# Performance work log

Measured on AMD Instinct MI355X. Metric: run time of the kernel, lower is better.

## Reference

```python
import jax, jax.numpy as jnp
import numpy as np

C = 512
NH = 8
DH = 64
GROUPS = 8
EPS = 1e-5


def setup_inputs() -> dict:
    key = jax.random.key(0)
    ks = jax.random.split(key, 20)
    s = 0.02
    d = {
        'x': jax.random.normal(ks[0], (16, C, 32, 32), jnp.float32),
        'gn_w': jnp.ones((C,), jnp.float32),
        'gn_b': jnp.zeros((C,), jnp.float32),
        'pin_w': jax.random.normal(ks[1], (C, C), jnp.float32) * s,
        'pin_b': jnp.zeros((C,), jnp.float32),
        'ln1_w': jnp.ones((C,), jnp.float32),
        'ln1_b': jnp.zeros((C,), jnp.float32),
        'wq': jax.random.normal(ks[2], (C, C), jnp.float32) * s,
        'wk': jax.random.normal(ks[3], (C, C), jnp.float32) * s,
        'wv': jax.random.normal(ks[4], (C, C), jnp.float32) * s,
        'wo': jax.random.normal(ks[5], (C, C), jnp.float32) * s,
        'bo': jnp.zeros((C,), jnp.float32),
        'ln3_w': jnp.ones((C,), jnp.float32),
        'ln3_b': jnp.zeros((C,), jnp.float32),
        'wg': jax.random.normal(ks[6], (C, 8 * C), jnp.float32) * s,
        'bg': jnp.zeros((8 * C,), jnp.float32),
        'wd': jax.random.normal(ks[7], (4 * C, C), jnp.float32) * s,
        'bd': jnp.zeros((C,), jnp.float32),
        'pout_w': jax.random.normal(ks[8], (C, C), jnp.float32) * s,
        'pout_b': jnp.zeros((C,), jnp.float32),
    }
    return d


def _group_norm(x, w, b):
    B, Cc, H, W = x.shape
    xg = x.reshape(B, GROUPS, Cc // GROUPS, H, W)
    mu = xg.mean(axis=(2, 3, 4), keepdims=True)
    var = xg.var(axis=(2, 3, 4), keepdims=True)
    xn = ((xg - mu) * jax.lax.rsqrt(var + EPS)).reshape(B, Cc, H, W)
    return xn * w[None, :, None, None] + b[None, :, None, None]


def _layer_norm(x, w, b):
    mu = x.mean(axis=-1, keepdims=True)
    var = x.var(axis=-1, keepdims=True)
    return (x - mu) * jax.lax.rsqrt(var + EPS) * w + b


def reference(x, gn_w, gn_b, pin_w, pin_b, ln1_w, ln1_b, wq, wk, wv, wo, bo,
              ln3_w, ln3_b, wg, bg, wd, bd, pout_w, pout_b):
    B, Cc, H, W = x.shape
    x_in = x
    h = _group_norm(x, gn_w, gn_b)
    # proj_in: 1x1 conv == channel matmul
    h = jnp.einsum('bchw,oc->bohw', h, pin_w) + pin_b[None, :, None, None]
    # [B, S, C] tokens
    t = h.reshape(B, Cc, H * W).transpose(0, 2, 1)
    # --- attention block ---
    tn = _layer_norm(t, ln1_w, ln1_b)
    S = H * W
    q = (tn @ wq).reshape(B, S, NH, DH)
    k = (tn @ wk).reshape(B, S, NH, DH)
    v = (tn @ wv).reshape(B, S, NH, DH)
    scale = DH ** -0.5
    scores = jnp.einsum('bshd,bthd->bhst', q, k) * scale  # [B,NH,S,S]
    wts = jax.nn.softmax(scores, axis=-1)
    attn = jnp.einsum('bhst,bthd->bshd', wts, v).reshape(B, S, Cc)
    t = attn @ wo + bo + t
    # --- GEGLU MLP ---
    tn = _layer_norm(t, ln3_w, ln3_b)
    hp = tn @ wg + bg
    a, g = hp[..., :4 * Cc], hp[..., 4 * Cc:]
    t = (a * jax.nn.gelu(g, approximate=False)) @ wd + bd + t
    # back to image
    h = t.transpose(0, 2, 1).reshape(B, Cc, H, W)
    out = jnp.einsum('bchw,oc->bohw', h, pout_w) + pout_b[None, :, None, None]
    return out + x_in
```

## Files before the change

### kernel.cpp

```cpp
#include <hip/hip_runtime.h>
#include <hip/hip_bf16.h>
#include <math.h>

typedef unsigned short u16;
typedef __attribute__((ext_vector_type(8))) short bf16x8;
typedef __attribute__((ext_vector_type(4))) float f32x4;

#define Bb 16
#define Cch 512
#define Ss 1024
#define NHh 8
#define DHh 64
#define CPG 64
#define EPSV 1e-5f
#define R_TOTAL (Bb*Ss)
#define QSCL 0.18033688011112042f

__device__ inline u16 f2bf(float f) {
    unsigned int u = __float_as_uint(f);
    unsigned int r = (u + 0x7fffu + ((u >> 16) & 1u)) >> 16;
    return (u16)r;
}
__device__ inline u16 f2bf_rz(float f) { return (u16)(__float_as_uint(f) >> 16); }
__device__ inline float bf2f(u16 v) { return __uint_as_float((unsigned)v << 16); }
__device__ inline float exp2_raw(float x) {
    float r; asm("v_exp_f32 %0, %1" : "=v"(r) : "v"(x)); return r;
}
__device__ inline float rcp_raw(float x) {
    float r; asm("v_rcp_f32 %0, %1" : "=v"(r) : "v"(x)); return r;
}
__device__ inline float gelu_f(float g) {
    float z = fabsf(g) * 0.70710678118654752f;
    float t = rcp_raw(1.0f + 0.3275911f * z);
    float poly = t * (0.254829592f + t * (-0.284496736f + t * (1.421413741f +
                 t * (-1.453152027f + t * 1.061405429f))));
    float e = exp2_raw(-z * z * 1.44269504089f);
    float erfa = 1.0f - poly * e;
    float erfv = (g < 0.f) ? -erfa : erfa;
    return 0.5f * g * (1.0f + erfv);
}

__device__ inline int swz(int row, int chunk) {
    return row * 64 + ((chunk ^ (row & 7)) * 8);
}
__device__ inline int psw(int row, int chunk) {
    return ((chunk >> 3) << 13) + row * 64 + (((chunk & 7) ^ (row & 7)) * 8);
}
__device__ inline int vsw(int row, int chunk) {
    return ((chunk >> 3) << 12) + row * 64 + (((chunk & 7) ^ (row & 7)) * 8);
}
__device__ inline int swzg(int r, int c) {
    int span = r >> 1;
    int c8 = ((r & 1) << 2) | c;
    return span * 64 + ((c8 ^ (span & 7)) * 8);
}

__global__ __launch_bounds__(256) void gn_stats(const float* __restrict__ x,
                                                float* __restrict__ stats) {
    int bg = blockIdx.x;
    int b = bg >> 3, g = bg & 7;
    const float4* base = (const float4*)(x + ((size_t)b * Cch + (size_t)g * CPG) * Ss);
    float s = 0.f, ss = 0.f;
    for (int i = threadIdx.x; i < CPG * Ss / 4; i += 256) {
        float4 v = base[i];
        s  += v.x + v.y + v.z + v.w;
        ss += v.x * v.x + v.y * v.y + v.z * v.z + v.w * v.w;
    }
    for (int o = 32; o > 0; o >>= 1) { s += __shfl_down(s, o); ss += __shfl_down(ss, o); }
    __shared__ float red[2][4];
    int wid = threadIdx.x >> 6, lane = threadIdx.x & 63;
    if (lane == 0) { red[0][wid] = s; red[1][wid] = ss; }
    __syncthreads();
    if (threadIdx.x == 0) {
        float S1 = red[0][0] + red[0][1] + red[0][2] + red[0][3];
        float S2 = red[1][0] + red[1][1] + red[1][2] + red[1][3];
        const float inv_n = 1.0f / (CPG * Ss);
        float mu = S1 * inv_n;
        float var = S2 * inv_n - mu * mu;
        stats[bg * 2]     = mu;
        stats[bg * 2 + 1] = rsqrtf(var + EPSV);
    }
}

__global__ __launch_bounds__(256) void gn_apply_t_bf(const float* __restrict__ x,
                                                     const float* __restrict__ stats,
                                                     const float* __restrict__ gw,
                                                     const float* __restrict__ gb,
                                                     u16* __restrict__ ht) {
    __shared__ float tile[32][33];
    int b  = blockIdx.z;
    int c0 = blockIdx.y * 32;
    int s0 = blockIdx.x * 32;
    int tx = threadIdx.x, ty = threadIdx.y;
#pragma unroll
    for (int i = 0; i < 4; i++) {
        int c = c0 + ty + i * 8;
        int g = c >> 6;
        float mu = stats[(b * 8 + g) * 2];
        float rs = stats[(b * 8 + g) * 2 + 1];
        float v = x[((size_t)b * Cch + c) * Ss + s0 + tx];
        tile[ty + i * 8][tx] = (v - mu) * rs * gw[c] + gb[c];
    }
    __syncthreads();
#pragma unroll
    for (int i = 0; i < 4; i++) {
        int s = s0 + ty + i * 8;
        ht[((size_t)b * Ss + s) * Cch + c0 + tx] = f2bf(tile[tx][ty + i * 8]);
    }
}

__global__ __launch_bounds__(256) void prep_all(const float* __restrict__ pin_w,
                                                const float* __restrict__ pout_w,
                                                u16* __restrict__ pinB,
                                                u16* __restrict__ poutB,
                                                const float* __restrict__ wq,
                                                const float* __restrict__ wk,
                                                const float* __restrict__ wv,
                                                const float* __restrict__ wo,
                                                u16* __restrict__ wqT,
                                                u16* __restrict__ wkT,
                                                u16* __restrict__ wvT,
                                                u16* __restrict__ woT,
                                                const float* __restrict__ wg,
                                                u16* __restrict__ wgT,
                                                const float* __restrict__ wd,
                                                u16* __restrict__ wdT) {
    __shared__ float tile[32][33];
    int bid = blockIdx.x;
    int tx = threadIdx.x, ty = threadIdx.y;
    int tid = ty * 32 + tx;
    if (bid < 512) {
        int base = bid * 1024 + tid * 4;
        const float* src; u16* dst; int off;
        if (base < 262144) { src = pin_w;  dst = pinB;  off = base; }
        else               { src = pout_w; dst = poutB; off = base - 262144; }
        float4 v = *(const float4*)&src[off];
        ushort4 o;
        o.x = f2bf(v.x); o.y = f2bf(v.y); o.z = f2bf(v.z); o.w = f2bf(v.w);
        *(ushort4*)&dst[off] = o;
        return;
    }
    const float* in; u16* outp; int c0, r0, C, R; float scl = 1.0f;
    if (bid < 1536) {
        int z = (bid - 512) >> 8, rem = (bid - 512) & 255;
        switch (z) {
            case 0: in = wq; outp = wqT; scl = QSCL; break;
            case 1: in = wk; outp = wkT; break;
            case 2: in = wv; outp = wvT; break;
            default: in = wo; outp = woT; break;
        }
        c0 = (rem & 15) * 32; r0 = (rem >> 4) * 32; C = 512; R = 512;
    } else if (bid < 3584) {
        int rem = bid - 1536;
        in = wg; outp = wgT; C = 4096; R = 512;
        c0 = (rem & 127) * 32; r0 = (rem >> 7) * 32;
    } else {
        int rem = bid - 3584;
        in = wd; outp = wdT; C = 512; R = 2048;
        c0 = (rem & 15) * 32; r0 = (rem >> 4) * 32;
    }
#pragma unroll
    for (int i = 0; i < 4; i++)
        tile[ty + i * 8][tx] = in[(size_t)(r0 + ty + i * 8) * C + c0 + tx] * scl;
    __syncthreads();
#pragma unroll
    for (int i = 0; i < 4; i++)
        outp[(size_t)(c0 + ty + i * 8) * R + r0 + tx] = f2bf(tile[tx][ty + i * 8]);
}

__global__ __launch_bounds__(256) void vtrans(const u16* __restrict__ in,
                                              u16* __restrict__ outp) {
    __shared__ u16 tile[64][66];
    int s0 = blockIdx.x * 64, h = blockIdx.y, b = blockIdx.z;
    const u16* src = in + ((size_t)b * Ss + s0) * Cch + h * 64;
    int r = threadIdx.x >> 3, c8 = (threadIdx.x & 7) * 8;
#pragma unroll
    for (int p = 0; p < 2; p++) {
        int rr = r + p * 32;
        *(int4*)&tile[rr][c8] = *(const int4*)&src[(size_t)rr * Cch + c8];
    }
    __syncthreads();
    u16* dst = outp + ((size_t)(b * 8 + h) * 64) * Ss + s0;
#pragma unroll
    for (int p = 0; p < 2; p++) {
        int d = r + p * 32;
        u16 vals[8];
#pragma unroll
        for (int e = 0; e < 8; e++) vals[e] = tile[c8 + e][d];
        *(int4*)&dst[(size_t)d * Ss + c8] = *(int4*)vals;
    }
}

__global__ __launch_bounds__(256) void layer_norm_rows_bf(const u16* __restrict__ in,
                                                          const float* __restrict__ w,
                                                          const float* __restrict__ bb,
                                                          u16* __restrict__ outp) {
    int row = blockIdx.x;
    const u16* p = in + (size_t)row * Cch;
    int i0 = threadIdx.x * 2;
    ushort2 u = *(const ushort2*)&p[i0];
    float v0 = bf2f(u.x), v1 = bf2f(u.y);
    float s = v0 + v1, ss = v0 * v0 + v1 * v1;
    for (int o = 32; o > 0; o >>= 1) { s += __shfl_down(s, o); ss += __shfl_down(ss, o); }
    __shared__ float red[2][4];
    __shared__ float mu_s, rs_s;
    int wid = threadIdx.x >> 6, lane = threadIdx.x & 63;
    if (lane == 0) { red[0][wid] = s; red[1][wid] = ss; }
    __syncthreads();
    if (threadIdx.x == 0) {
        float S1 = red[0][0] + red[0][1] + red[0][2] + red[0][3];
        float S2 = red[1][0] + red[1][1] + red[1][2] + red[1][3];
        float mu = S1 * (1.0f / Cch);
        float var = S2 * (1.0f / Cch) - mu * mu;
        mu_s = mu; rs_s = rsqrtf(var + EPSV);
    }
    __syncthreads();
    float mu = mu_s, rs = rs_s;
    outp[(size_t)row * Cch + i0]     = f2bf((v0 - mu) * rs * w[i0] + bb[i0]);
    outp[(size_t)row * Cch + i0 + 1] = f2bf((v1 - mu) * rs * w[i0 + 1] + bb[i0 + 1]);
}

template<int EPI>
__global__ __launch_bounds__(512) void mfma_gemm(const u16* __restrict__ A,
                                                 const u16* __restrict__ Bt,
                                                 const float* __restrict__ bias,
                                                 float* __restrict__ fout,
                                                 u16* __restrict__ outb,
                                                 int K, int N) {
    __shared__ u16 As[256 * 32];
    __shared__ u16 Bs[128 * 32];
    int tid = threadIdx.x;
    int m0 = blockIdx.y * 256, n0 = blockIdx.x * 128;
    int wave = tid >> 6, lane = tid & 63;
    int wr = wave >> 1, wc = wave & 1;
    int l15 = lane & 15, l4 = lane >> 4;

    f32x4 zero4 = {0.f, 0.f, 0.f, 0.f};
    f32x4 acc[4][4];
#pragma unroll
    for (int i = 0; i < 4; i++)
#pragma unroll
        for (int j = 0; j < 4; j++) acc[i][j] = zero4;

    int srow = tid >> 1;
    int sc0  = (tid & 1) * 2;
    int se   = sc0 * 8;
    int brow = tid >> 2;
    int bch  = tid & 3;
    int bqe  = bch * 8;

    int4 ra0, ra1, rb0;
    {
        const u16* pa = A  + (size_t)(m0 + srow) * K + se;
        ra0 = *(const int4*)pa; ra1 = *(const int4*)(pa + 8);
        rb0 = *(const int4*)(Bt + (size_t)(n0 + brow) * K + bqe);
    }
    for (int kt = 0; kt < K; kt += 32) {
        __syncthreads();
        *(int4*)&As[swzg(srow, sc0)]     = ra0;
        *(int4*)&As[swzg(srow, sc0 + 1)] = ra1;
        *(int4*)&Bs[swzg(brow, bch)]     = rb0;
        __syncthreads();
        int kn = kt + 32;
        if (kn < K) {
            const u16* pa = A  + (size_t)(m0 + srow) * K + kn + se;
            ra0 = *(const int4*)pa; ra1 = *(const int4*)(pa + 8);
            rb0 = *(const int4*)(Bt + (size_t)(n0 + brow) * K + kn + bqe);
        }
        bf16x8 af[4], bfr[4];
#pragma unroll
        for (int mi = 0; mi < 4; mi++)
            af[mi] = *(const bf16x8*)&As[swzg(wr * 64 + mi * 16 + l15, l4)];
#pragma unroll
        for (int nj = 0; nj < 4; nj++)
            bfr[nj] = *(const bf16x8*)&Bs[swzg(wc * 64 + nj * 16 + l15, l4)];
#pragma unroll
        for (int mi = 0; mi < 4; mi++)
#pragma unroll
            for (int nj = 0; nj < 4; nj++)
                acc[mi][nj] = __builtin_amdgcn_mfma_f32_16x16x32_bf16(af[mi], bfr[nj], acc[mi][nj], 0, 0, 0);
    }

#pragma unroll
    for (int mi = 0; mi < 4; mi++)
#pragma unroll
        for (int nj = 0; nj < 4; nj++)
#pragma unroll
            for (int r = 0; r < 4; r++) {
                int row = m0 + wr * 64 + mi * 16 + l4 * 4 + r;
                int col = n0 + wc * 64 + nj * 16 + l15;
                float v = acc[mi][nj][r];
                if constexpr (EPI == 0) {
                    outb[(size_t)row * N + col] = f2bf(v);
                } else if constexpr (EPI == 1) {
                    fout[(size_t)row * N + col] = v + bias[col];
                } else if constexpr (EPI == 6) {
                    outb[(size_t)row * N + col] = f2bf(v + bias[col]);
                } else if constexpr (EPI == 7) {
                    size_t idx = (size_t)row * N + col;
                    v += bias[col] + bf2f(outb[idx]);
                    outb[idx] = f2bf(v);
                } else if constexpr (EPI == 8) {
                    size_t idx = (size_t)(col >> 9) * 8388608 + (size_t)row * 512 + (col & 511);
                    outb[idx] = f2bf(v);
                }
            }
}

__global__ __launch_bounds__(512) void geglu_mfma(const u16* __restrict__ A,
                                                  const u16* __restrict__ WgT,
                                                  const float* __restrict__ bg,
                                                  u16* __restrict__ ag) {
    __shared__ u16 As[256 * 32];
    __shared__ u16 Bs1[64 * 32];
    __shared__ u16 Bs2[64 * 32];
    const int K = 512;
    int tid = threadIdx.x;
    int m0 = blockIdx.y * 256, n0 = blockIdx.x * 64;
    int wave = tid >> 6, lane = tid & 63;
    int wr = wave >> 1, wc = wave & 1;
    int l15 = lane & 15, l4 = lane >> 4;

    f32x4 zero4 = {0.f, 0.f, 0.f, 0.f};
    f32x4 accA[4][2], accG[4][2];
#pragma unroll
    for (int i = 0; i < 4; i++) { accA[i][0] = zero4; accA[i][1] = zero4; accG[i][0] = zero4; accG[i][1] = zero4; }

    int srow = tid >> 1;
    int sc0  = (tid & 1) * 2;
    int se   = sc0 * 8;
    int bsel = tid >> 8;
    int bt   = tid & 255;
    int brow = bt >> 2;
    int bch  = bt & 3;
    int bqe  = bch * 8;
    const u16* gbp = WgT + (size_t)(bsel * 2048 + n0 + brow) * K + bqe;

    int4 ra0, ra1, rb;
    {
        const u16* pa = A + (size_t)(m0 + srow) * K + se;
        ra0 = *(const int4*)pa; ra1 = *(const int4*)(pa + 8);
        rb = *(const int4*)gbp;
    }
    for (int kt = 0; kt < K; kt += 32) {
        __syncthreads();
        *(int4*)&As[swzg(srow, sc0)]     = ra0;
        *(int4*)&As[swzg(srow, sc0 + 1)] = ra1;
        if (bsel == 0) *(int4*)&Bs1[swzg(brow, bch)] = rb;
        else           *(int4*)&Bs2[swzg(brow, bch)] = rb;
        __syncthreads();
        int kn = kt + 32;
        if (kn < K) {
            const u16* pa = A + (size_t)(m0 + srow) * K + kn + se;
            ra0 = *(const int4*)pa; ra1 = *(const int4*)(pa + 8);
            rb = *(const int4*)(gbp + kn);
        }
        bf16x8 af[4], b1[2], b2[2];
#pragma unroll
        for (int mi = 0; mi < 4; mi++)
            af[mi] = *(const bf16x8*)&As[swzg(wr * 64 + mi * 16 + l15, l4)];
#pragma unroll
        for (int nj = 0; nj < 2; nj++) {
            b1[nj] = *(const bf16x8*)&Bs1[swzg(wc * 32 + nj * 16 + l15, l4)];
            b2[nj] = *(const bf16x8*)&Bs2[swzg(wc * 32 + nj * 16 + l15, l4)];
        }
#pragma unroll
        for (int mi = 0; mi < 4; mi++)
#pragma unroll
            for (int nj = 0; nj < 2; nj++) {
                accA[mi][nj] = __builtin_amdgcn_mfma_f32_16x16x32_bf16(af[mi], b1[nj], accA[mi][nj], 0, 0, 0);
                accG[mi][nj] = __builtin_amdgcn_mfma_f32_16x16x32_bf16(af[mi], b2[nj], accG[mi][nj], 0, 0, 0);
            }
    }

#pragma unroll
    for (int mi = 0; mi < 4; mi++)
#pragma unroll
        for (int nj = 0; nj < 2; nj++)
#pragma unroll
            for (int r = 0; r < 4; r++) {
                int row = m0 + wr * 64 + mi * 16 + l4 * 4 + r;
                int col = n0 + wc * 32 + nj * 16 + l15;
                float a = accA[mi][nj][r] + bg[col];
                float g = accG[mi][nj][r] + bg[2048 + col];
                ag[(size_t)row * 2048 + col] = f2bf(a * gelu_f(g));
            }
}

__global__ __launch_bounds__(512) void flash_attn_mfma(const u16* __restrict__ q,
                                                       const u16* __restrict__ k,
                                                       const u16* __restrict__ vt,
                                                       u16* __restrict__ o) {
    __shared__ u16 Ps[2 * 128 * 64];
    __shared__ u16 Ks[128 * 64];
    __shared__ u16 Vt[2 * 64 * 64];
    const int tid = threadIdx.x;
    const int h = blockIdx.x, b = blockIdx.z;
    const int q0 = blockIdx.y * 128;
    const size_t hb  = (size_t)b * Ss * Cch + (size_t)h * DHh;
    const size_t vhb = ((size_t)(b * NHh + h) * DHh) * Ss;

    const int wq = tid >> 6;
    const int lane = tid & 63;
    const int l15 = lane & 15, l4 = lane >> 4;

    const int kr = tid >> 2, kc = (tid & 3) * 2;
    const int vf = tid >> 8, vtn = tid & 255;
    const int vd = vtn >> 2, vc = (vtn & 3) * 2;
    const u16* kbase = k + hb + (size_t)kr * Cch + (size_t)kc * 8;
    const u16* vbase = vt + vhb + (size_t)vd * Ss + vf * 64 + (size_t)vc * 8;

    {
        int r = tid >> 2, ch = (tid & 3) * 2;
        const u16* src = q + hb + (size_t)(q0 + r) * Cch;
        *(int4*)&Ps[psw(r, ch)]     = *(const int4*)(src + ch * 8);
        *(int4*)&Ps[psw(r, ch + 1)] = *(const int4*)(src + (ch + 1) * 8);
    }
    __syncthreads();
    bf16x8 aq[2];
    aq[0] = *(const bf16x8*)&Ps[psw(wq * 16 + l15, 0 * 4 + l4)];
    aq[1] = *(const bf16x8*)&Ps[psw(wq * 16 + l15, 1 * 4 + l4)];

    f32x4 zero4 = {0.f, 0.f, 0.f, 0.f};
    f32x4 oacc[4];
    float m_[4], l_[4];
#pragma unroll
    for (int j = 0; j < 4; j++) oacc[j] = zero4;
#pragma unroll
    for (int r = 0; r < 4; r++) { m_[r] = -1e30f; l_[r] = 0.f; }

    int4 rk0, rk1, rv0, rv1;
    rk0 = *(const int4*)(kbase);
    rk1 = *(const int4*)(kbase + 8);
    rv0 = *(const int4*)(vbase);
    rv1 = *(const int4*)(vbase + 8);

    for (int t0 = 0; t0 < Ss; t0 += 128) {
        __syncthreads();
        *(int4*)&Ks[swz(kr, kc)]     = rk0;
        *(int4*)&Ks[swz(kr, kc + 1)] = rk1;
        *(int4*)&Vt[vsw(vd, vf * 8 + vc)]     = rv0;
        *(int4*)&Vt[vsw(vd, vf * 8 + vc + 1)] = rv1;
        __syncthreads();
        if (t0 + 128 < Ss) {
            rk0 = *(const int4*)(kbase + (size_t)(t0 + 128) * Cch);
            rk1 = *(const int4*)(kbase + (size_t)(t0 + 128) * Cch + 8);
            rv0 = *(const int4*)(vbase + t0 + 128);
            rv1 = *(const int4*)(vbase + t0 + 128 + 8);
        }

        f32x4 sacc[8];
#pragma unroll
        for (int j = 0; j < 8; j++) sacc[j] = zero4;
#pragma unroll
        for (int ks = 0; ks < 2; ks++) {
#pragma unroll
            for (int j = 0; j < 8; j++) {
                bf16x8 bk = *(const bf16x8*)&Ks[swz(j * 16 + l15, ks * 4 + l4)];
                sacc[j] = __builtin_amdgcn_mfma_f32_16x16x32_bf16(aq[ks], bk, sacc[j], 0, 0, 0);
            }
        }

        float tmv[4];
        int grew = 0;
#pragma unroll
        for (int r = 0; r < 4; r++) {
            float tm = fmaxf(fmaxf(fmaxf(sacc[0][r], sacc[1][r]), fmaxf(sacc[2][r], sacc[3][r])),
                             fmaxf(fmaxf(sacc[4][r], sacc[5][r]), fmaxf(sacc[6][r], sacc[7][r])));
            tm = fmaxf(tm, __shfl_xor(tm, 1));
            tm = fmaxf(tm, __shfl_xor(tm, 2));
            tm = fmaxf(tm, __shfl_xor(tm, 4));
            tm = fmaxf(tm, __shfl_xor(tm, 8));
            tmv[r] = tm;
            grew |= (tm > m_[r]);
        }

        if (__any(grew)) {
#pragma unroll
            for (int r = 0; r < 4; r++) {
                float nm = fmaxf(m_[r], tmv[r]);
                float sc = exp2_raw(m_[r] - nm);
                m_[r] = nm;
                int row = wq * 16 + l4 * 4 + r;
                int rx = row & 7, b64 = row * 64, wi = l15 & 7, hi = l15 >> 3;
                float rs = 0.f;
#pragma unroll
                for (int j = 0; j < 8; j++) {
                    float p = exp2_raw(sacc[j][r] - nm);
                    int cnk = 2 * j + hi;
                    Ps[((cnk >> 3) << 13) + b64 + (((cnk & 7) ^ rx) * 8) + wi] = f2bf_rz(p);
                    rs += p;
                }
                l_[r] = l_[r] * sc + rs;
#pragma unroll
                for (int j = 0; j < 4; j++) oacc[j][r] *= sc;
            }
        } else {
#pragma unroll
            for (int r = 0; r < 4; r++) {
                float nm = m_[r];
                int row = wq * 16 + l4 * 4 + r;
                int rx = row & 7, b64 = row * 64, wi = l15 & 7, hi = l15 >> 3;
                float rs = 0.f;
#pragma unroll
                for (int j = 0; j < 8; j++) {
                    float p = exp2_raw(sacc[j][r] - nm);
                    int cnk = 2 * j + hi;
                    Ps[((cnk >> 3) << 13) + b64 + (((cnk & 7) ^ rx) * 8) + wi] = f2bf_rz(p);
                    rs += p;
                }
                l_[r] += rs;
            }
        }

#pragma unroll
        for (int ks = 0; ks < 4; ks++) {
            bf16x8 pa = *(const bf16x8*)&Ps[psw(wq * 16 + l15, ks * 4 + l4)];
#pragma unroll
            for (int j = 0; j < 4; j++) {
                bf16x8 bv = *(const bf16x8*)&Vt[vsw(j * 16 + l15, ks * 4 + l4)];
                oacc[j] = __builtin_amdgcn_mfma_f32_16x16x32_bf16(pa, bv, oacc[j], 0, 0, 0);
            }
        }
    }

#pragma unroll
    for (int r = 0; r < 4; r++) {
        float lt = l_[r];
        lt += __shfl_xor(lt, 1);
        lt += __shfl_xor(lt, 2);
        lt += __shfl_xor(lt, 4);
        lt += __shfl_xor(lt, 8);
        float inv = 1.0f / lt;
        int row = wq * 16 + l4 * 4 + r;
        int rx = row & 7, b64 = row * 64, wi = l15 & 7, hi = l15 >> 3;
#pragma unroll
        for (int j = 0; j < 4; j++) {
            int cnk = 2 * j + hi;
            Ps[b64 + ((cnk ^ rx) * 8) + wi] = f2bf(oacc[j][r] * inv);
        }
    }
    __syncthreads();
    {
        int r = tid >> 2, ch = (tid & 3) * 2;
        u16* dst = o + hb + (size_t)(q0 + r) * Cch;
        *(int4*)(dst + ch * 8)       = *(const int4*)&Ps[psw(r, ch)];
        *(int4*)(dst + (ch + 1) * 8) = *(const int4*)&Ps[psw(r, ch + 1)];
    }
}

__global__ __launch_bounds__(256) void final_out_bf(const u16* __restrict__ tmp,
                                                    const float* __restrict__ x,
                                                    float* __restrict__ outp) {
    __shared__ float tile[32][33];
    int b = blockIdx.z, c0 = blockIdx.y * 32, s0 = blockIdx.x * 32;
    int tx = threadIdx.x, ty = threadIdx.y;
#pragma unroll
    for (int i = 0; i < 4; i++) {
        int s = s0 + ty + i * 8;
        tile[ty + i * 8][tx] = bf2f(tmp[((size_t)b * Ss + s) * Cch + c0 + tx]);
    }
    __syncthreads();
#pragma unroll
    for (int i = 0; i < 4; i++) {
        int c = c0 + ty + i * 8;
        size_t idx = ((size_t)b * Cch + c) * Ss + s0 + tx;
        outp[idx] = tile[tx][ty + i * 8] + x[idx];
    }
}

extern "C" void kernel_launch(void* const* d_in, const int* in_sizes, int n_in,
                              void* d_out, int out_size, void* d_ws, size_t ws_size,
                              hipStream_t stream) {
    (void)in_sizes; (void)n_in; (void)out_size; (void)ws_size;
    const float* x      = (const float*)d_in[0];
    const float* gn_w   = (const float*)d_in[1];
    const float* gn_b   = (const float*)d_in[2];
    const float* pin_w  = (const float*)d_in[3];
    const float* pin_b  = (const float*)d_in[4];
    const float* ln1_w  = (const float*)d_in[5];
    const float* ln1_b  = (const float*)d_in[6];
    const float* wq     = (const float*)d_in[7];
    const float* wk     = (const float*)d_in[8];
    const float* wv     = (const float*)d_in[9];
    const float* wo     = (const float*)d_in[10];
    const float* bo     = (const float*)d_in[11];
    const float* ln3_w  = (const float*)d_in[12];
    const float* ln3_b  = (const float*)d_in[13];
    const float* wg     = (const float*)d_in[14];
    const float* bg     = (const float*)d_in[15];
    const float* wd     = (const float*)d_in[16];
    const float* bd     = (const float*)d_in[17];
    const float* pout_w = (const float*)d_in[18];
    const float* pout_b = (const float*)d_in[19];
    float* out = (float*)d_out;

    char* W = (char*)d_ws;
    u16* tb        = (u16*)W;
    float* tmp_f32 = (float*)(W + 33554432);
    u16* qb    = (u16*)(W + 67108864);
    u16* kb    = qb + 8388608;
    u16* vb    = kb + 8388608;
    u16* attnb = vb + 8388608;
    u16* Xb    = attnb + 8388608;
    float* stats = (float*)(W + 67108864 + 5ull * 16777216);
    u16* wbase = (u16*)(W + 67108864 + 5ull * 16777216 + 1024);
    u16* pinB  = wbase;
    u16* poutB = pinB  + 262144;
    u16* wqT   = poutB + 262144;
    u16* wkT   = wqT   + 262144;
    u16* wvT   = wkT   + 262144;
    u16* woT   = wvT   + 262144;
    u16* wgT   = woT   + 262144;
    u16* wdT   = wgT   + 2097152;
    u16* ag    = qb;
    u16* vtb   = (u16*)tmp_f32;

    dim3 tb8(32, 8);

    gn_stats<<<128, 256, 0, stream>>>(x, stats);
    prep_all<<<4608, tb8, 0, stream>>>(pin_w, pout_w, pinB, poutB,
                                       wq, wk, wv, wo, wqT, wkT, wvT, woT,
                                       wg, wgT, wd, wdT);

    gn_apply_t_bf<<<dim3(32, 16, 16), tb8, 0, stream>>>(x, stats, gn_w, gn_b, Xb);

    mfma_gemm<6><<<dim3(4, 64), 512, 0, stream>>>(Xb, pinB, pin_b, nullptr, tb, 512, 512);
    layer_norm_rows_bf<<<16384, 256, 0, stream>>>(tb, ln1_w, ln1_b, Xb);
    mfma_gemm<8><<<dim3(12, 64), 512, 0, stream>>>(Xb, wqT, nullptr, nullptr, qb, 512, 1536);
    vtrans<<<dim3(16, 8, 16), 256, 0, stream>>>(vb, vtb);
    flash_attn_mfma<<<dim3(8, 8, 16), 512, 0, stream>>>(qb, kb, vtb, attnb);
    mfma_gemm<7><<<dim3(4, 64), 512, 0, stream>>>(attnb, woT, bo, nullptr, tb, 512, 512);
    layer_norm_rows_bf<<<16384, 256, 0, stream>>>(tb, ln3_w, ln3_b, Xb);
    geglu_mfma<<<dim3(32, 64), 512, 0, stream>>>(Xb, wgT, bg, ag);
    mfma_gemm<7><<<dim3(4, 64), 512, 0, stream>>>(ag, wdT, bd, nullptr, tb, 2048, 512);
    mfma_gemm<6><<<dim3(4, 64), 512, 0, stream>>>(tb, poutB, pout_b, nullptr, Xb, 512, 512);
    final_out_bf<<<dim3(32, 16, 16), tb8, 0, stream>>>(Xb, x, out);
}
```

Before: 422.0 us.

## Double-buffer shared memory tiles in MFMA GEMM to drop a barrier per k-step

```diff
diff --git a/kernel.cpp b/kernel.cpp
--- a/kernel.cpp
+++ b/kernel.cpp
@@ -227,8 +227,8 @@
                                                  float* __restrict__ fout,
                                                  u16* __restrict__ outb,
                                                  int K, int N) {
-    __shared__ u16 As[256 * 32];
-    __shared__ u16 Bs[128 * 32];
+    __shared__ u16 As[2][256 * 32];
+    __shared__ u16 Bs[2][128 * 32];
     int tid = threadIdx.x;
     int m0 = blockIdx.y * 256, n0 = blockIdx.x * 128;
     int wave = tid >> 6, lane = tid & 63;
@@ -249,36 +249,46 @@
     int bch  = tid & 3;
     int bqe  = bch * 8;
 
-    int4 ra0, ra1, rb0;
-    {
-        const u16* pa = A  + (size_t)(m0 + srow) * K + se;
-        ra0 = *(const int4*)pa; ra1 = *(const int4*)(pa + 8);
-        rb0 = *(const int4*)(Bt + (size_t)(n0 + brow) * K + bqe);
-    }
+    const u16* pa = A  + (size_t)(m0 + srow) * K + se;
+    const u16* pb = Bt + (size_t)(n0 + brow) * K + bqe;
+
+    int4 ra0 = *(const int4*)pa;
+    int4 ra1 = *(const int4*)(pa + 8);
+    int4 rb0 = *(const int4*)pb;
+    *(int4*)&As[0][swzg(srow, sc0)]     = ra0;
+    *(int4*)&As[0][swzg(srow, sc0 + 1)] = ra1;
+    *(int4*)&Bs[0][swzg(brow, bch)]     = rb0;
+    ra0 = *(const int4*)(pa + 32);
+    ra1 = *(const int4*)(pa + 40);
+    rb0 = *(const int4*)(pb + 32);
+    __syncthreads();
+
+    int p = 0;
     for (int kt = 0; kt < K; kt += 32) {
-        __syncthreads();
-        *(int4*)&As[swzg(srow, sc0)]     = ra0;
-        *(int4*)&As[swzg(srow, sc0 + 1)] = ra1;
-        *(int4*)&Bs[swzg(brow, bch)]     = rb0;
-        __syncthreads();
-        int kn = kt + 32;
-        if (kn < K) {
-            const u16* pa = A  + (size_t)(m0 + srow) * K + kn + se;
-            ra0 = *(const int4*)pa; ra1 = *(const int4*)(pa + 8);
-            rb0 = *(const int4*)(Bt + (size_t)(n0 + brow) * K + kn + bqe);
-        }
         bf16x8 af[4], bfr[4];
 #pragma unroll
         for (int mi = 0; mi < 4; mi++)
-            af[mi] = *(const bf16x8*)&As[swzg(wr * 64 + mi * 16 + l15, l4)];
+            af[mi] = *(const bf16x8*)&As[p][swzg(wr * 64 + mi * 16 + l15, l4)];
 #pragma unroll
         for (int nj = 0; nj < 4; nj++)
-            bfr[nj] = *(const bf16x8*)&Bs[swzg(wc * 64 + nj * 16 + l15, l4)];
+            bfr[nj] = *(const bf16x8*)&Bs[p][swzg(wc * 64 + nj * 16 + l15, l4)];
 #pragma unroll
         for (int mi = 0; mi < 4; mi++)
 #pragma unroll
             for (int nj = 0; nj < 4; nj++)
                 acc[mi][nj] = __builtin_amdgcn_mfma_f32_16x16x32_bf16(af[mi], bfr[nj], acc[mi][nj], 0, 0, 0);
+        if (kt + 32 < K) {
+            *(int4*)&As[p ^ 1][swzg(srow, sc0)]     = ra0;
+            *(int4*)&As[p ^ 1][swzg(srow, sc0 + 1)] = ra1;
+            *(int4*)&Bs[p ^ 1][swzg(brow, bch)]     = rb0;
+            if (kt + 64 < K) {
+                ra0 = *(const int4*)(pa + kt + 64);
+                ra1 = *(const int4*)(pa + kt + 72);
+                rb0 = *(const int4*)(pb + kt + 64);
+            }
+        }
+        __syncthreads();
+        p ^= 1;
     }
 
 #pragma unroll
```

New measurement: 406.2 us. 3.7% less time.

## Double-buffer LDS tiles in MFMA GEMM with two-stage register prefetch

Applied to the files above, without the earlier changes.

```diff
diff --git a/kernel.cpp b/kernel.cpp
--- a/kernel.cpp
+++ b/kernel.cpp
@@ -221,14 +221,14 @@
 }
 
 template<int EPI>
-__global__ __launch_bounds__(512) void mfma_gemm(const u16* __restrict__ A,
-                                                 const u16* __restrict__ Bt,
-                                                 const float* __restrict__ bias,
-                                                 float* __restrict__ fout,
-                                                 u16* __restrict__ outb,
-                                                 int K, int N) {
-    __shared__ u16 As[256 * 32];
-    __shared__ u16 Bs[128 * 32];
+__global__ __launch_bounds__(512, 2) void mfma_gemm(const u16* __restrict__ A,
+                                                    const u16* __restrict__ Bt,
+                                                    const float* __restrict__ bias,
+                                                    float* __restrict__ fout,
+                                                    u16* __restrict__ outb,
+                                                    int K, int N) {
+    __shared__ u16 As[2][256 * 32];
+    __shared__ u16 Bs[2][128 * 32];
     int tid = threadIdx.x;
     int m0 = blockIdx.y * 256, n0 = blockIdx.x * 128;
     int wave = tid >> 6, lane = tid & 63;
@@ -249,36 +249,72 @@
     int bch  = tid & 3;
     int bqe  = bch * 8;
 
-    int4 ra0, ra1, rb0;
-    {
-        const u16* pa = A  + (size_t)(m0 + srow) * K + se;
-        ra0 = *(const int4*)pa; ra1 = *(const int4*)(pa + 8);
-        rb0 = *(const int4*)(Bt + (size_t)(n0 + brow) * K + bqe);
-    }
-    for (int kt = 0; kt < K; kt += 32) {
+    const u16* pa = A  + (size_t)(m0 + srow) * K + se;
+    const u16* pb = Bt + (size_t)(n0 + brow) * K + bqe;
+
+    int4 sa0 = *(const int4*)pa;
+    int4 sa1 = *(const int4*)(pa + 8);
+    int4 sb0 = *(const int4*)pb;
+    *(int4*)&As[0][swzg(srow, sc0)]     = sa0;
+    *(int4*)&As[0][swzg(srow, sc0 + 1)] = sa1;
+    *(int4*)&Bs[0][swzg(brow, bch)]     = sb0;
+    int4 ta0 = *(const int4*)(pa + 32);
+    int4 ta1 = *(const int4*)(pa + 40);
+    int4 tb0 = *(const int4*)(pb + 32);
+    sa0 = *(const int4*)(pa + 64);
+    sa1 = *(const int4*)(pa + 72);
+    sb0 = *(const int4*)(pb + 64);
+    __syncthreads();
+
+    for (int kt = 0; kt < K; kt += 64) {
+        {
+            bf16x8 af[4], bfr[4];
+#pragma unroll
+            for (int mi = 0; mi < 4; mi++)
+                af[mi] = *(const bf16x8*)&As[0][swzg(wr * 64 + mi * 16 + l15, l4)];
+#pragma unroll
+            for (int nj = 0; nj < 4; nj++)
+                bfr[nj] = *(const bf16x8*)&Bs[0][swzg(wc * 64 + nj * 16 + l15, l4)];
+#pragma unroll
+            for (int mi = 0; mi < 4; mi++)
+#pragma unroll
+                for (int nj = 0; nj < 4; nj++)
+                    acc[mi][nj] = __builtin_amdgcn_mfma_f32_16x16x32_bf16(af[mi], bfr[nj], acc[mi][nj], 0, 0, 0);
+        }
+        *(int4*)&As[1][swzg(srow, sc0)]     = ta0;
+        *(int4*)&As[1][swzg(srow, sc0 + 1)] = ta1;
+        *(int4*)&Bs[1][swzg(brow, bch)]     = tb0;
+        if (kt + 96 < K) {
+            ta0 = *(const int4*)(pa + kt + 96);
+            ta1 = *(const int4*)(pa + kt + 104);
+            tb0 = *(const int4*)(pb + kt + 96);
+        }
         __syncthreads();
-        *(int4*)&As[swzg(srow, sc0)]     = ra0;
-        *(int4*)&As[swzg(srow, sc0 + 1)] = ra1;
-        *(int4*)&Bs[swzg(brow, bch)]     = rb0;
-        __syncthreads();
-        int kn = kt + 32;
-        if (kn < K) {
-            const u16* pa = A  + (size_t)(m0 + srow) * K + kn + se;
-            ra0 = *(const int4*)pa; ra1 = *(const int4*)(pa + 8);
-            rb0 = *(const int4*)(Bt + (size_t)(n0 + brow) * K + kn + bqe);
-        }
-        bf16x8 af[4], bfr[4];
-#pragma unroll
-        for (int mi = 0; mi < 4; mi++)
-            af[mi] = *(const bf16x8*)&As[swzg(wr * 64 + mi * 16 + l15, l4)];
-#pragma unroll
-        for (int nj = 0; nj < 4; nj++)
-            bfr[nj] = *(const bf16x8*)&Bs[swzg(wc * 64 + nj * 16 + l15, l4)];
-#pragma unroll
-        for (int mi = 0; mi < 4; mi++)
+        {
+            bf16x8 af[4], bfr[4];
+#pragma unroll
+            for (int mi = 0; mi < 4; mi++)
+                af[mi] = *(const bf16x8*)&As[1][swzg(wr * 64 + mi * 16 + l15, l4)];
 #pragma unroll
             for (int nj = 0; nj < 4; nj++)
-                acc[mi][nj] = __builtin_amdgcn_mfma_f32_16x16x32_bf16(af[mi], bfr[nj], acc[mi][nj], 0, 0, 0);
+                bfr[nj] = *(const bf16x8*)&Bs[1][swzg(wc * 64 + nj * 16 + l15, l4)];
+#pragma unroll
+            for (int mi = 0; mi < 4; mi++)
+#pragma unroll
+                for (int nj = 0; nj < 4; nj++)
+                    acc[mi][nj] = __builtin_amdgcn_mfma_f32_16x16x32_bf16(af[mi], bfr[nj], acc[mi][nj], 0, 0, 0);
+        }
+        if (kt + 64 < K) {
+            *(int4*)&As[0][swzg(srow, sc0)]     = sa0;
+            *(int4*)&As[0][swzg(srow, sc0 + 1)] = sa1;
+            *(int4*)&Bs[0][swzg(brow, bch)]     = sb0;
+            if (kt + 128 < K) {
+                sa0 = *(const int4*)(pa + kt + 128);
+                sa1 = *(const int4*)(pa + kt + 136);
+                sb0 = *(const int4*)(pb + kt + 128);
+            }
+            __syncthreads();
+        }
     }
 
 #pragma unroll
```

New measurement: 412.2 us. 1.02x faster.
